# Kernel tuning notes

Measured on AMD Instinct MI355X. Metric: run time of the kernel, lower is better.

Reference implementation:

```python
import jax, jax.numpy as jnp
import numpy as np

DIM = 192; D_STATE = 16; D_CONV = 4; EXPAND = 2
D_INNER = EXPAND * DIM          # 384
DT_RANK = -(-DIM // 16)         # ceil(192/16) = 12
BSZ, T, H, W = 1, 16, 64, 64


def setup_inputs() -> dict:
    key = jax.random.key(0)
    ks = jax.random.split(key, 10)
    s = 0.02
    return {
        "x": jax.random.normal(ks[0], (BSZ, DIM, T, H, W), jnp.float32),
        "ln1_g": jnp.ones((DIM,), jnp.float32),
        "ln1_b": jnp.zeros((DIM,), jnp.float32),
        "ln2_g": jnp.ones((DIM,), jnp.float32),
        "ln2_b": jnp.zeros((DIM,), jnp.float32),
        "W_in": jax.random.normal(ks[1], (2 * D_INNER, DIM), jnp.float32) * s,
        "conv_w": jax.random.normal(ks[2], (D_INNER, D_CONV), jnp.float32) * 0.3,
        "conv_b": jnp.zeros((D_INNER,), jnp.float32),
        "W_xp": jax.random.normal(ks[3], (DT_RANK + 2 * D_STATE, D_INNER), jnp.float32) * s,
        "W_dt": jax.random.normal(ks[4], (D_INNER, DT_RANK), jnp.float32) * 0.1,
        "b_dt": jax.random.normal(ks[5], (D_INNER,), jnp.float32) * 0.1 - 4.0,
        "A_log": jnp.log(jnp.broadcast_to(jnp.arange(1, D_STATE + 1, dtype=jnp.float32), (D_INNER, D_STATE))),
        "D": jnp.ones((D_INNER,), jnp.float32),
        "W_out": jax.random.normal(ks[6], (DIM, D_INNER), jnp.float32) * s,
    }


def _layer_norm(x, g, b, eps=1e-5):
    m = x.mean(-1, keepdims=True)
    v = ((x - m) ** 2).mean(-1, keepdims=True)
    return (x - m) * jax.lax.rsqrt(v + eps) * g + b


def _mamba(tokens, W_in, conv_w, conv_b, W_xp, W_dt, b_dt, A_log, D, W_out):
    B, L, _ = tokens.shape
    xz = tokens @ W_in.T                      # (B, L, 2*d_inner)
    xc, z = jnp.split(xz, 2, axis=-1)
    # causal depthwise conv1d along L
    xin = xc.transpose(0, 2, 1)               # (B, d_inner, L)
    xconv = jax.lax.conv_general_dilated(
        xin, conv_w[:, None, :], (1,), [(D_CONV - 1, 0)],
        dimension_numbers=("NCH", "OIH", "NCH"), feature_group_count=D_INNER)
    xconv = xconv + conv_b[None, :, None]
    xs = jax.nn.silu(xconv.transpose(0, 2, 1))  # (B, L, d_inner)
    x_dbl = xs @ W_xp.T                        # (B, L, dt_rank + 2*d_state)
    dt, Bm, Cm = jnp.split(x_dbl, [DT_RANK, DT_RANK + D_STATE], axis=-1)
    dt = jax.nn.softplus(dt @ W_dt.T + b_dt)   # (B, L, d_inner)
    A = -jnp.exp(A_log)                        # (d_inner, d_state)
    dA = jnp.exp(dt[..., None] * A)            # (B, L, d_inner, d_state)
    dBx = dt[..., None] * Bm[:, :, None, :] * xs[..., None]

    def step(h, inp):
        dA_t, dBx_t, C_t = inp
        h = dA_t * h + dBx_t                   # (B, d_inner, d_state)
        return h, jnp.einsum("bds,bs->bd", h, C_t)

    h0 = jnp.zeros((B, D_INNER, D_STATE), tokens.dtype)
    _, ys = jax.lax.scan(step, h0, (dA.transpose(1, 0, 2, 3),
                                    dBx.transpose(1, 0, 2, 3),
                                    Cm.transpose(1, 0, 2)))
    y = ys.transpose(1, 0, 2) + xs * D         # (B, L, d_inner)
    y = y * jax.nn.silu(z)
    return y @ W_out.T                          # (B, L, dim)


def reference(x, ln1_g, ln1_b, ln2_g, ln2_b, W_in, conv_w, conv_b,
              W_xp, W_dt, b_dt, A_log, D, W_out):
    B, C, T_, H_, W_ = x.shape
    Hs, Ws = H_ // 4, W_ // 4
    # avg_pool3d kernel=(1,4,4) stride=(1,4,4)
    x_ds = x.reshape(B, C, T_, Hs, 4, Ws, 4).mean((4, 6))
    tokens = x_ds.reshape(B, C, T_ * Hs * Ws).transpose(0, 2, 1)  # (B, L, C)
    y = _layer_norm(tokens, ln1_g, ln1_b)
    y = _mamba(y, W_in, conv_w, conv_b, W_xp, W_dt, b_dt, A_log, D, W_out)
    out = _layer_norm(tokens + y, ln2_g, ln2_b)                    # (B, L, C)
    out5 = out.transpose(0, 2, 1).reshape(B, C, T_, Hs, Ws)
    pooled = out5.mean((3, 4))                                     # (B, C, T)
    mag = jnp.abs(jnp.fft.rfft(pooled, axis=2))
    weight = jax.nn.sigmoid(mag[:, :, 1:8].mean(-1))               # (B, C)
    out5 = out5 * weight[:, :, None, None, None]
    up = jax.image.resize(out5, (B, C, T_, H_, W_), method="trilinear")
    return up * jax.nn.sigmoid(x)
```

## Files before the change

kernel.cpp:

```cpp
#include <hip/hip_runtime.h>
#include <math.h>

#define DIMC 192
#define DI   384
#define DS   16
#define LTOK 4096
#define NCH  256
#define CLEN 16
#define NLANE (DI*DS)
#define L2E  1.4426950408889634f
#define LN2  0.6931471805599453f

typedef __attribute__((ext_vector_type(8))) short    bf16x8;
typedef __attribute__((ext_vector_type(8))) unsigned short u16x8;
typedef __attribute__((ext_vector_type(4))) float    f32x4;

__device__ __forceinline__ float EXP2(float x) { return __builtin_amdgcn_exp2f(x); }
__device__ __forceinline__ float RCP(float x)  { return __builtin_amdgcn_rcpf(x); }
__device__ __forceinline__ float LOG2(float x) { return __builtin_amdgcn_logf(x); }

__device__ __forceinline__ float sigmoidf_(float x) { return RCP(1.f + EXP2(-x * L2E)); }
__device__ __forceinline__ float siluf_(float x)    { return x * RCP(1.f + EXP2(-x * L2E)); }
__device__ __forceinline__ unsigned short f2bf(float f) {
    unsigned int u = __float_as_uint(f);
    u += 0x7FFFu + ((u >> 16) & 1u);
    return (unsigned short)(u >> 16);
}
__device__ __forceinline__ float bf2f(unsigned short b) {
    return __uint_as_float(((unsigned int)b) << 16);
}

__global__ __launch_bounds__(256) void poolln_kernel(const float* __restrict__ x,
                                                     const float* __restrict__ g,
                                                     const float* __restrict__ bb,
                                                     const float* __restrict__ W_in,
                                                     const float* __restrict__ W_out,
                                                     const float* __restrict__ W_xp,
                                                     const float* __restrict__ A_log,
                                                     float* __restrict__ tokens,
                                                     unsigned short* __restrict__ ytok,
                                                     unsigned short* __restrict__ W_in_bf,
                                                     unsigned short* __restrict__ W_out_bf,
                                                     unsigned short* __restrict__ W_xp_pad,
                                                     float* __restrict__ A2pre) {
    int blk = blockIdx.x;
    int tid = threadIdx.x;
    if (blk >= 256) {
        int id = (blk - 256) * 256 + tid;
        for (int i = id; i < 768 * 192; i += 8192) W_in_bf[i] = f2bf(W_in[i]);
        for (int i = id; i < 192 * 384; i += 8192) W_out_bf[i] = f2bf(W_out[i]);
        for (int i = id; i < 64 * 384; i += 8192) {
            int row = i / 384;
            W_xp_pad[i] = (row < 44) ? f2bf(W_xp[i]) : (unsigned short)0;
        }
        for (int i = id; i < NLANE; i += 8192) A2pre[i] = -expf(A_log[i]) * L2E;
        return;
    }
    int t = blk >> 4, hs = blk & 15;
    int grp = tid >> 4, ws = tid & 15;
    __shared__ float P[16 * 196];
    __shared__ float ms[16], rs[16];
    #pragma unroll
    for (int k = 0; k < 12; ++k) {
        int c = grp + (k << 4);
        const float* base = x + ((size_t)(c * 16 + t) * 64 + hs * 4) * 64 + ws * 4;
        float s = 0.f;
        #pragma unroll
        for (int i = 0; i < 4; ++i) {
            float4 v = *(const float4*)(base + i * 64);
            s += v.x + v.y + v.z + v.w;
        }
        P[ws * 196 + c] = s * 0.0625f;
    }
    __syncthreads();
    float s1 = 0.f, s2 = 0.f;
    #pragma unroll
    for (int k = 0; k < 12; ++k) {
        float v = P[grp * 196 + ws + 16 * k];
        s1 += v; s2 += v * v;
    }
    s1 += __shfl_xor(s1, 1); s2 += __shfl_xor(s2, 1);
    s1 += __shfl_xor(s1, 2); s2 += __shfl_xor(s2, 2);
    s1 += __shfl_xor(s1, 4); s2 += __shfl_xor(s2, 4);
    s1 += __shfl_xor(s1, 8); s2 += __shfl_xor(s2, 8);
    if (ws == 0) {
        float m = s1 * (1.f / 192.f);
        ms[grp] = m;
        rs[grp] = rsqrtf(s2 * (1.f / 192.f) - m * m + 1e-5f);
    }
    __syncthreads();
    int l0 = t * 256 + hs * 16;
    for (int e = tid; e < 16 * 192; e += 256) {
        int w2 = e / 192, c = e - w2 * 192;
        float v = P[w2 * 196 + c];
        float val = (v - ms[w2]) * rs[w2] * g[c] + bb[c];
        tokens[(size_t)(l0 + w2) * DIMC + c] = v;
        ytok[(size_t)(l0 + w2) * DIMC + c] = f2bf(val);
    }
}

template<int K>
__global__ __launch_bounds__(256) void gemm_mfma(const unsigned short* __restrict__ A,
                                                 const unsigned short* __restrict__ Wb,
                                                 float* __restrict__ Cout,
                                                 int N) {
    constexpr int KT = 192;
    constexpr int KP = KT + 8;
    __shared__ unsigned short As[64 * KP];
    __shared__ unsigned short Bs[64 * KP];
    int bm = blockIdx.y * 64;
    int bn = blockIdx.x * 64;
    int tid = threadIdx.x;
    int lane = tid & 63, w = tid >> 6;
    int wr = w >> 1, wc = w & 1;
    int r16 = lane & 15, h = lane >> 4;
    f32x4 acc[2][2] = {};
    for (int kt = 0; kt < K; kt += KT) {
        for (int c = tid; c < 64 * (KT / 8); c += 256) {
            int row = c / (KT / 8), col = (c % (KT / 8)) * 8;
            *(u16x8*)&As[row * KP + col] = *(const u16x8*)(A + (size_t)(bm + row) * K + kt + col);
            *(u16x8*)&Bs[row * KP + col] = *(const u16x8*)(Wb + (size_t)(bn + row) * K + kt + col);
        }
        __syncthreads();
        #pragma unroll
        for (int k0 = 0; k0 < KT; k0 += 32) {
            bf16x8 a0 = *(const bf16x8*)&As[(wr * 32 + r16)      * KP + k0 + 8 * h];
            bf16x8 a1 = *(const bf16x8*)&As[(wr * 32 + 16 + r16) * KP + k0 + 8 * h];
            bf16x8 b0 = *(const bf16x8*)&Bs[(wc * 32 + r16)      * KP + k0 + 8 * h];
            bf16x8 b1 = *(const bf16x8*)&Bs[(wc * 32 + 16 + r16) * KP + k0 + 8 * h];
            acc[0][0] = __builtin_amdgcn_mfma_f32_16x16x32_bf16(a0, b0, acc[0][0], 0, 0, 0);
            acc[0][1] = __builtin_amdgcn_mfma_f32_16x16x32_bf16(a0, b1, acc[0][1], 0, 0, 0);
            acc[1][0] = __builtin_amdgcn_mfma_f32_16x16x32_bf16(a1, b0, acc[1][0], 0, 0, 0);
            acc[1][1] = __builtin_amdgcn_mfma_f32_16x16x32_bf16(a1, b1, acc[1][1], 0, 0, 0);
        }
        __syncthreads();
    }
    #pragma unroll
    for (int fm = 0; fm < 2; ++fm)
        #pragma unroll
        for (int fn = 0; fn < 2; ++fn)
            #pragma unroll
            for (int i = 0; i < 4; ++i) {
                int r = bm + wr * 32 + fm * 16 + h * 4 + i;
                int cc = bn + wc * 32 + fn * 16 + r16;
                Cout[(size_t)r * N + cc] = acc[fm][fn][i];
            }
}

__global__ __launch_bounds__(256) void convxdbl(const float* __restrict__ xz,
                                                const float* __restrict__ conv_w,
                                                const float* __restrict__ conv_b,
                                                const unsigned short* __restrict__ Wxp,
                                                unsigned short* __restrict__ xsb,
                                                float* __restrict__ x_dbl) {
    int l0 = blockIdx.x * 16;
    int tid = threadIdx.x;
    __shared__ unsigned short As[16 * 392];
    __shared__ float xd[16 * 64];
    for (int e = tid * 2; e < 16 * 384; e += 512) {
        int row = e / 384, d = e - row * 384;
        int l = l0 + row;
        float ax = conv_b[d], ay = conv_b[d + 1];
        #pragma unroll
        for (int k = 0; k < 4; ++k) {
            int ll = l - 3 + k;
            if (ll >= 0) {
                float2 v = *(const float2*)(xz + (size_t)ll * 768 + d);
                ax = fmaf(conv_w[d * 4 + k],       v.x, ax);
                ay = fmaf(conv_w[(d + 1) * 4 + k], v.y, ay);
            }
        }
        ushort2 b2;
        b2.x = f2bf(siluf_(ax));
        b2.y = f2bf(siluf_(ay));
        *(ushort2*)&As[row * 392 + d] = b2;
        *(ushort2*)(xsb + (size_t)l * 384 + d) = b2;
    }
    __syncthreads();
    int lane = tid & 63, w = tid >> 6;
    int r16 = lane & 15, hh = lane >> 4;
    f32x4 acc = {};
    #pragma unroll
    for (int k0 = 0; k0 < 384; k0 += 32) {
        bf16x8 a = *(const bf16x8*)&As[r16 * 392 + k0 + 8 * hh];
        bf16x8 b = *(const bf16x8*)(Wxp + (size_t)(w * 16 + r16) * 384 + k0 + 8 * hh);
        acc = __builtin_amdgcn_mfma_f32_16x16x32_bf16(a, b, acc, 0, 0, 0);
    }
    #pragma unroll
    for (int i = 0; i < 4; ++i) xd[(hh * 4 + i) * 64 + w * 16 + r16] = acc[i];
    __syncthreads();
    {
        int e = tid * 4;
        int row = e >> 6, col = e & 63;
        *(float4*)(x_dbl + (size_t)(l0 + row) * 64 + col) = *(const float4*)&xd[e];
    }
}

__global__ __launch_bounds__(256) void scan1(const float* __restrict__ x_dbl,
                                             const unsigned short* __restrict__ xsb,
                                             const float* __restrict__ W_dt,
                                             const float* __restrict__ b_dt,
                                             const float* __restrict__ A2pre,
                                             float* __restrict__ chA,
                                             float* __restrict__ chB,
                                             float* __restrict__ Dloc,
                                             unsigned short* __restrict__ yloc) {
    int tid = threadIdx.x;
    int dg = blockIdx.x;
    int c  = blockIdx.y;
    __shared__ float xdblS[16 * 48];
    __shared__ float wdtS[64 * 13];
    __shared__ float dtS[16][64];
    __shared__ unsigned short xsS[16][64];
    for (int i = tid; i < 768; i += 256) {
        int row = i / 48, col = i - row * 48;
        xdblS[i] = x_dbl[(size_t)(c * 16 + row) * 64 + col];
    }
    for (int i = tid; i < 768; i += 256) {
        int dl_ = i / 12, r = i - dl_ * 12;
        wdtS[dl_ * 13 + r] = W_dt[(size_t)dg * 768 + i];
    }
    for (int i = tid; i < 1024; i += 256) {
        int row = i >> 6, dl_ = i & 63;
        xsS[row][dl_] = xsb[(size_t)(c * 16 + row) * 384 + dg * 64 + dl_];
    }
    __syncthreads();
    {
        int dl_ = tid & 63;
        float bd = b_dt[dg * 64 + dl_];
        #pragma unroll
        for (int i2 = 0; i2 < 4; ++i2) {
            int row = (tid >> 6) + 4 * i2;
            float s = bd;
            #pragma unroll
            for (int r = 0; r < 12; ++r)
                s = fmaf(xdblS[row * 48 + r], wdtS[dl_ * 13 + r], s);
            dtS[row][dl_] = (s > 20.f) ? s : LOG2(1.f + EXP2(s * L2E)) * LN2;
        }
    }
    __syncthreads();
    int sq = tid & 3, dl = tid >> 2;
    int d = dg * 64 + dl;
    float4 a4 = *(const float4*)(A2pre + (size_t)d * DS + sq * 4);
    float A2[4] = {a4.x, a4.y, a4.z, a4.w};
    float h[4] = {};
    float dts = 0.f;
    #pragma unroll
    for (int i = 0; i < CLEN; ++i) {
        int l = c * CLEN + i;
        float dtv = dtS[i][dl];
        float xv  = bf2f(xsS[i][dl]);
        float dtx = dtv * xv;
        dts += dtv;
        float y = 0.f;
        #pragma unroll
        for (int u = 0; u < 4; ++u) {
            float a = EXP2(dtv * A2[u]);
            h[u] = fmaf(a, h[u], dtx * xdblS[i * 48 + 12 + sq * 4 + u]);
            y = fmaf(h[u], xdblS[i * 48 + 28 + sq * 4 + u], y);
        }
        y += __shfl_xor(y, 1);
        y += __shfl_xor(y, 2);
        if (sq == 0) {
            yloc[(size_t)l * DI + d] = f2bf(y);
            Dloc[(size_t)l * DI + d] = dts;
        }
    }
    size_t base = (size_t)c * NLANE + d * DS + sq * 4;
    float4 pa, pb;
    pa.x = EXP2(dts * A2[0]); pa.y = EXP2(dts * A2[1]);
    pa.z = EXP2(dts * A2[2]); pa.w = EXP2(dts * A2[3]);
    pb.x = h[0]; pb.y = h[1]; pb.z = h[2]; pb.w = h[3];
    *(float4*)&chA[base] = pa;
    *(float4*)&chB[base] = pb;
}

__global__ __launch_bounds__(256) void scan2p(const float* __restrict__ chA,
                                              const float* __restrict__ chB,
                                              float* __restrict__ hst) {
    int tid = threadIdx.x;
    int ll = tid & 15;
    int g  = tid >> 4;
    int lane = blockIdx.x * 16 + ll;
    float a[16], b[16];
    #pragma unroll
    for (int i = 0; i < 16; ++i) {
        int c = g * 16 + i;
        a[i] = chA[(size_t)c * NLANE + lane];
        b[i] = chB[(size_t)c * NLANE + lane];
    }
    float Ath = 1.f, Bth = 0.f;
    #pragma unroll
    for (int i = 0; i < 16; ++i) {
        Bth = fmaf(a[i], Bth, b[i]);
        Ath *= a[i];
    }
    __shared__ float sA[16][17], sB[16][17];
    sA[g][ll] = Ath; sB[g][ll] = Bth;
    __syncthreads();
    #pragma unroll
    for (int step = 1; step < 16; step <<= 1) {
        float pA = 1.f, pB = 0.f;
        if (g >= step) { pA = sA[g - step][ll]; pB = sB[g - step][ll]; }
        __syncthreads();
        if (g >= step) {
            float cA = sA[g][ll], cB = sB[g][ll];
            sA[g][ll] = cA * pA;
            sB[g][ll] = fmaf(cA, pB, cB);
        }
        __syncthreads();
    }
    float h = (g == 0) ? 0.f : sB[g - 1][ll];
    #pragma unroll
    for (int i = 0; i < 16; ++i) {
        int c = g * 16 + i;
        hst[(size_t)c * NLANE + lane] = h;
        h = fmaf(a[i], h, b[i]);
    }
}

__global__ __launch_bounds__(256) void scan3fix(const float* __restrict__ hst,
                                                const float* __restrict__ Dloc,
                                                const float* __restrict__ x_dbl,
                                                const float* __restrict__ A2pre,
                                                const unsigned short* __restrict__ xsb,
                                                const float* __restrict__ xz,
                                                const float* __restrict__ Dvec,
                                                unsigned short* __restrict__ ybuf) {
    int dg = blockIdx.x;
    int c  = blockIdx.y;
    int tid = threadIdx.x;
    int ll = tid >> 4, dl = tid & 15;
    int d = dg * 16 + dl;
    int l = c * 16 + ll;
    __shared__ float hpS[16][17];
    __shared__ float A2S[16][17];
    __shared__ float CsS[256];
    {
        int dd = tid >> 4, ss = tid & 15;
        hpS[dd][ss] = hst[(size_t)c * NLANE + dg * 256 + tid];
        A2S[dd][ss] = A2pre[(size_t)dg * 256 + tid];
        CsS[tid]    = x_dbl[(size_t)(c * 16 + dd) * 64 + 28 + ss];
    }
    __syncthreads();
    float Dl = Dloc[(size_t)l * DI + d];
    float y  = bf2f(ybuf[(size_t)l * DI + d]);
    float xv = bf2f(xsb[(size_t)l * DI + d]);
    float z  = xz[(size_t)l * 768 + 384 + d];
    #pragma unroll
    for (int s = 0; s < 16; ++s) {
        float e = EXP2(A2S[dl][s] * Dl);
        y = fmaf(CsS[ll * 16 + s] * e, hpS[dl][s], y);
    }
    float val = (y + xv * Dvec[d]) * siluf_(z);
    ybuf[(size_t)l * DI + d] = f2bf(val);
}

__global__ __launch_bounds__(256) void ln2_kernel(const float* __restrict__ tokens,
                                                  const float* __restrict__ gout,
                                                  const float* __restrict__ g,
                                                  const float* __restrict__ bb,
                                                  float* __restrict__ o5) {
    int blk = blockIdx.x;
    int t = blk >> 4, g16 = blk & 15;
    int l0 = t * 256 + g16 * 16;
    int tid = threadIdx.x;
    __shared__ float P[16 * 196];
    __shared__ float ms[16], rs[16];
    for (int e = tid; e < 3072; e += 256) {
        int w2 = e / 192, c = e - w2 * 192;
        size_t off = (size_t)(l0 + w2) * DIMC + c;
        P[w2 * 196 + c] = tokens[off] + gout[off];
    }
    __syncthreads();
    int grp = tid >> 4, ws = tid & 15;
    float s1 = 0.f, s2 = 0.f;
    #pragma unroll
    for (int k = 0; k < 12; ++k) {
        float v = P[grp * 196 + ws + 16 * k];
        s1 += v; s2 += v * v;
    }
    s1 += __shfl_xor(s1, 1); s2 += __shfl_xor(s2, 1);
    s1 += __shfl_xor(s1, 2); s2 += __shfl_xor(s2, 2);
    s1 += __shfl_xor(s1, 4); s2 += __shfl_xor(s2, 4);
    s1 += __shfl_xor(s1, 8); s2 += __shfl_xor(s2, 8);
    if (ws == 0) {
        float m = s1 * (1.f / 192.f);
        ms[grp] = m;
        rs[grp] = rsqrtf(s2 * (1.f / 192.f) - m * m + 1e-5f);
    }
    __syncthreads();
    for (int e = tid; e < 3072; e += 256) {
        int c = e >> 4, w2 = e & 15;
        float val = (P[w2 * 196 + c] - ms[w2]) * rs[w2] * g[c] + bb[c];
        o5[((size_t)c * 16 + t) * 256 + g16 * 16 + w2] = val;
    }
}

__global__ __launch_bounds__(256) void fft_kernel(const float* __restrict__ o5,
                                                  float* __restrict__ wgt) {
    int c = blockIdx.x;
    __shared__ float pooled[16];
    __shared__ float mag[8];
    int tid = threadIdx.x;
    int wv = tid >> 6, lane = tid & 63;
    for (int t = wv * 4; t < wv * 4 + 4; ++t) {
        float s = 0.f;
        #pragma unroll
        for (int r = 0; r < 4; ++r) s += o5[(size_t)c * 4096 + t * 256 + lane + r * 64];
        s += __shfl_xor(s, 1); s += __shfl_xor(s, 2); s += __shfl_xor(s, 4);
        s += __shfl_xor(s, 8); s += __shfl_xor(s, 16); s += __shfl_xor(s, 32);
        if (lane == 0) pooled[t] = s * (1.f / 256.f);
    }
    __syncthreads();
    if (tid >= 1 && tid <= 7) {
        int k = tid;
        float re = 0.f, im = 0.f;
        for (int t = 0; t < 16; ++t) {
            float ang = -0.39269908169872414f * (float)(k * t);
            re = fmaf(pooled[t], cosf(ang), re);
            im = fmaf(pooled[t], sinf(ang), im);
        }
        mag[k] = sqrtf(re * re + im * im);
    }
    __syncthreads();
    if (tid == 0) {
        float m = 0.f;
        for (int k = 1; k <= 7; ++k) m += mag[k];
        wgt[c] = sigmoidf_(m * (1.f / 7.f));
    }
}

__global__ __launch_bounds__(256) void upsample_kernel(const float* __restrict__ o5,
                                                       const float* __restrict__ wgt,
                                                       const float* __restrict__ x,
                                                       float* __restrict__ out) {
    int idx = blockIdx.x * 256 + threadIdx.x;
    int k  = idx & 15;
    int h  = (idx >> 4) & 63;
    int t  = (idx >> 10) & 15;
    int c  = idx >> 14;
    float sh = h * 0.25f - 0.375f;
    int h0 = (int)floorf(sh); float fh = sh - (float)h0;
    int h0c = min(max(h0, 0), 15), h1c = min(max(h0 + 1, 0), 15);
    const float* pl = o5 + ((size_t)c * 16 + t) * 256;
    int cm = max(k - 1, 0), cp = min(k + 1, 15);
    float r0m = pl[h0c * 16 + cm], r00 = pl[h0c * 16 + k], r0p = pl[h0c * 16 + cp];
    float r1m = pl[h1c * 16 + cm], r10 = pl[h1c * 16 + k], r1p = pl[h1c * 16 + cp];
    float gh = 1.f - fh;
    float vm = r0m * gh + r1m * fh;
    float v0 = r00 * gh + r10 * fh;
    float vp = r0p * gh + r1p * fh;
    float wc = wgt[c];
    size_t off = (size_t)idx * 4;
    float4 xv = *(const float4*)(x + off);
    float4 o;
    o.x = (vm * 0.375f + v0 * 0.625f) * wc * sigmoidf_(xv.x);
    o.y = (vm * 0.125f + v0 * 0.875f) * wc * sigmoidf_(xv.y);
    o.z = (v0 * 0.875f + vp * 0.125f) * wc * sigmoidf_(xv.z);
    o.w = (v0 * 0.625f + vp * 0.375f) * wc * sigmoidf_(xv.w);
    *(float4*)(out + off) = o;
}

extern "C" void kernel_launch(void* const* d_in, const int* in_sizes, int n_in,
                              void* d_out, int out_size, void* d_ws, size_t ws_size,
                              hipStream_t stream) {
    const float* x      = (const float*)d_in[0];
    const float* ln1_g  = (const float*)d_in[1];
    const float* ln1_b  = (const float*)d_in[2];
    const float* ln2_g  = (const float*)d_in[3];
    const float* ln2_b  = (const float*)d_in[4];
    const float* W_in   = (const float*)d_in[5];
    const float* conv_w = (const float*)d_in[6];
    const float* conv_b = (const float*)d_in[7];
    const float* W_xp   = (const float*)d_in[8];
    const float* W_dt   = (const float*)d_in[9];
    const float* b_dt   = (const float*)d_in[10];
    const float* A_log  = (const float*)d_in[11];
    const float* Dvec   = (const float*)d_in[12];
    const float* W_out  = (const float*)d_in[13];
    float* out = (float*)d_out;

    float* ws = (float*)d_ws;
    float* tokens = ws;  ws += (size_t)LTOK * DIMC;
    float* xz     = ws;  ws += (size_t)LTOK * 768;
    float* x_dbl  = ws;  ws += (size_t)LTOK * 64;
    float* chA    = ws;  ws += (size_t)NLANE * NCH;
    float* chB    = ws;  ws += (size_t)NLANE * NCH;
    float* hst    = ws;  ws += (size_t)NLANE * NCH;
    float* Dloc   = ws;  ws += (size_t)LTOK * DI;
    float* gout   = ws;  ws += (size_t)LTOK * DIMC;
    float* o5     = ws;  ws += (size_t)DIMC * LTOK;
    float* A2pre  = ws;  ws += NLANE;
    float* wgt    = ws;  ws += 256;
    unsigned short* ytok     = (unsigned short*)ws;  ws += (size_t)LTOK * DIMC / 2;
    unsigned short* ybuf     = (unsigned short*)ws;  ws += (size_t)LTOK * DI / 2;
    unsigned short* xsb      = (unsigned short*)ws;  ws += (size_t)LTOK * DI / 2;
    unsigned short* W_in_bf  = (unsigned short*)ws;  ws += (size_t)768 * 192 / 2;
    unsigned short* W_out_bf = (unsigned short*)ws;  ws += (size_t)192 * 384 / 2;
    unsigned short* W_xp_pad = (unsigned short*)ws;  ws += (size_t)64 * 384 / 2;

    poolln_kernel<<<288, 256, 0, stream>>>(x, ln1_g, ln1_b, W_in, W_out, W_xp, A_log,
                                           tokens, ytok, W_in_bf, W_out_bf, W_xp_pad, A2pre);
    gemm_mfma<192><<<dim3(12, 64), 256, 0, stream>>>(ytok, W_in_bf, xz, 768);
    convxdbl<<<256, 256, 0, stream>>>(xz, conv_w, conv_b, W_xp_pad, xsb, x_dbl);
    scan1<<<dim3(6, NCH), 256, 0, stream>>>(x_dbl, xsb, W_dt, b_dt, A2pre, chA, chB, Dloc, ybuf);
    scan2p<<<NLANE / 16, 256, 0, stream>>>(chA, chB, hst);
    scan3fix<<<dim3(24, NCH), 256, 0, stream>>>(hst, Dloc, x_dbl, A2pre, xsb, xz, Dvec, ybuf);
    gemm_mfma<384><<<dim3(3, 64), 256, 0, stream>>>(ybuf, W_out_bf, gout, 192);
    ln2_kernel<<<256, 256, 0, stream>>>(tokens, gout, ln2_g, ln2_b, o5);
    fft_kernel<<<192, 256, 0, stream>>>(o5, wgt);
    upsample_kernel<<<12288, 256, 0, stream>>>(o5, wgt, x, out);
}
```

Before: 116.0 us.

## Fuse conv+xproj with chunk scan, out-GEMM with LN2, and FFT with upsample

Merges the conv/x-projection kernel with the first scan pass into one 384-thread block per chunk, where each thread owns one channel and all 16 states, so x_dbl and xs are reused from shared memory. It also fuses the output projection GEMM with the residual-add and second LayerNorm, which drops the gout buffer. The per-channel FFT gating is recomputed inside each upsample block, removing two launches and the wgt buffer. In exchange, the scan gets fewer and larger blocks (256 blocks), the gemmln kernel runs only 64 blocks, and the pooled FFT work is repeated 16 times per channel.

```diff
diff --git a/kernel.cpp b/kernel.cpp
--- a/kernel.cpp
+++ b/kernel.cpp
@@ -147,132 +147,113 @@
             }
 }
 
-__global__ __launch_bounds__(256) void convxdbl(const float* __restrict__ xz,
+__global__ __launch_bounds__(384) void convscan(const float* __restrict__ xz,
                                                 const float* __restrict__ conv_w,
                                                 const float* __restrict__ conv_b,
                                                 const unsigned short* __restrict__ Wxp,
+                                                const float* __restrict__ W_dt,
+                                                const float* __restrict__ b_dt,
+                                                const float* __restrict__ A2pre,
                                                 unsigned short* __restrict__ xsb,
-                                                float* __restrict__ x_dbl) {
-    int l0 = blockIdx.x * 16;
+                                                float* __restrict__ x_dbl,
+                                                float* __restrict__ chA,
+                                                float* __restrict__ chB,
+                                                float* __restrict__ Dloc,
+                                                unsigned short* __restrict__ yloc) {
+    int c = blockIdx.x;
+    int l0 = c * CLEN;
     int tid = threadIdx.x;
     __shared__ unsigned short As[16 * 392];
     __shared__ float xd[16 * 64];
-    for (int e = tid * 2; e < 16 * 384; e += 512) {
-        int row = e / 384, d = e - row * 384;
-        int l = l0 + row;
-        float ax = conv_b[d], ay = conv_b[d + 1];
-        #pragma unroll
-        for (int k = 0; k < 4; ++k) {
-            int ll = l - 3 + k;
-            if (ll >= 0) {
-                float2 v = *(const float2*)(xz + (size_t)ll * 768 + d);
-                ax = fmaf(conv_w[d * 4 + k],       v.x, ax);
-                ay = fmaf(conv_w[(d + 1) * 4 + k], v.y, ay);
-            }
-        }
-        ushort2 b2;
-        b2.x = f2bf(siluf_(ax));
-        b2.y = f2bf(siluf_(ay));
-        *(ushort2*)&As[row * 392 + d] = b2;
-        *(ushort2*)(xsb + (size_t)l * 384 + d) = b2;
-    }
-    __syncthreads();
-    int lane = tid & 63, w = tid >> 6;
-    int r16 = lane & 15, hh = lane >> 4;
-    f32x4 acc = {};
-    #pragma unroll
-    for (int k0 = 0; k0 < 384; k0 += 32) {
-        bf16x8 a = *(const bf16x8*)&As[r16 * 392 + k0 + 8 * hh];
-        bf16x8 b = *(const bf16x8*)(Wxp + (size_t)(w * 16 + r16) * 384 + k0 + 8 * hh);
-        acc = __builtin_amdgcn_mfma_f32_16x16x32_bf16(a, b, acc, 0, 0, 0);
-    }
-    #pragma unroll
-    for (int i = 0; i < 4; ++i) xd[(hh * 4 + i) * 64 + w * 16 + r16] = acc[i];
-    __syncthreads();
     {
-        int e = tid * 4;
-        int row = e >> 6, col = e & 63;
-        *(float4*)(x_dbl + (size_t)(l0 + row) * 64 + col) = *(const float4*)&xd[e];
-    }
-}
-
-__global__ __launch_bounds__(256) void scan1(const float* __restrict__ x_dbl,
-                                             const unsigned short* __restrict__ xsb,
-                                             const float* __restrict__ W_dt,
-                                             const float* __restrict__ b_dt,
-                                             const float* __restrict__ A2pre,
-                                             float* __restrict__ chA,
-                                             float* __restrict__ chB,
-                                             float* __restrict__ Dloc,
-                                             unsigned short* __restrict__ yloc) {
-    int tid = threadIdx.x;
-    int dg = blockIdx.x;
-    int c  = blockIdx.y;
-    __shared__ float xdblS[16 * 48];
-    __shared__ float wdtS[64 * 13];
-    __shared__ float dtS[16][64];
-    __shared__ unsigned short xsS[16][64];
-    for (int i = tid; i < 768; i += 256) {
-        int row = i / 48, col = i - row * 48;
-        xdblS[i] = x_dbl[(size_t)(c * 16 + row) * 64 + col];
-    }
-    for (int i = tid; i < 768; i += 256) {
-        int dl_ = i / 12, r = i - dl_ * 12;
-        wdtS[dl_ * 13 + r] = W_dt[(size_t)dg * 768 + i];
-    }
-    for (int i = tid; i < 1024; i += 256) {
-        int row = i >> 6, dl_ = i & 63;
-        xsS[row][dl_] = xsb[(size_t)(c * 16 + row) * 384 + dg * 64 + dl_];
-    }
-    __syncthreads();
-    {
-        int dl_ = tid & 63;
-        float bd = b_dt[dg * 64 + dl_];
-        #pragma unroll
-        for (int i2 = 0; i2 < 4; ++i2) {
-            int row = (tid >> 6) + 4 * i2;
-            float s = bd;
-            #pragma unroll
-            for (int r = 0; r < 12; ++r)
-                s = fmaf(xdblS[row * 48 + r], wdtS[dl_ * 13 + r], s);
-            dtS[row][dl_] = (s > 20.f) ? s : LOG2(1.f + EXP2(s * L2E)) * LN2;
-        }
-    }
-    __syncthreads();
-    int sq = tid & 3, dl = tid >> 2;
-    int d = dg * 64 + dl;
-    float4 a4 = *(const float4*)(A2pre + (size_t)d * DS + sq * 4);
-    float A2[4] = {a4.x, a4.y, a4.z, a4.w};
-    float h[4] = {};
+        int d = tid;
+        float cw0 = conv_w[d * 4 + 0], cw1 = conv_w[d * 4 + 1];
+        float cw2 = conv_w[d * 4 + 2], cw3 = conv_w[d * 4 + 3];
+        float cb = conv_b[d];
+        float xv[19];
+        #pragma unroll
+        for (int j = 0; j < 19; ++j) {
+            int ll = l0 - 3 + j;
+            xv[j] = (ll >= 0) ? xz[(size_t)ll * 768 + d] : 0.f;
+        }
+        #pragma unroll
+        for (int i = 0; i < 16; ++i) {
+            float a = cb;
+            a = fmaf(cw0, xv[i], a);
+            a = fmaf(cw1, xv[i + 1], a);
+            a = fmaf(cw2, xv[i + 2], a);
+            a = fmaf(cw3, xv[i + 3], a);
+            As[i * 392 + d] = f2bf(siluf_(a));
+        }
+    }
+    __syncthreads();
+    #pragma unroll
+    for (int k = 0; k < 16; ++k)
+        xsb[(size_t)(l0 + k) * DI + tid] = As[k * 392 + tid];
+    if (tid < 256) {
+        int lane = tid & 63, w = tid >> 6;
+        int r16 = lane & 15, hh = lane >> 4;
+        f32x4 acc = {};
+        #pragma unroll
+        for (int k0 = 0; k0 < 384; k0 += 32) {
+            bf16x8 a = *(const bf16x8*)&As[r16 * 392 + k0 + 8 * hh];
+            bf16x8 b = *(const bf16x8*)(Wxp + (size_t)(w * 16 + r16) * 384 + k0 + 8 * hh);
+            acc = __builtin_amdgcn_mfma_f32_16x16x32_bf16(a, b, acc, 0, 0, 0);
+        }
+        #pragma unroll
+        for (int i = 0; i < 4; ++i) xd[(hh * 4 + i) * 64 + w * 16 + r16] = acc[i];
+    }
+    __syncthreads();
+    if (tid < 256) {
+        int row = tid >> 6, col = (tid & 63) * 4;
+        *(float4*)(x_dbl + (size_t)(l0 + row) * 64 + col) = *(const float4*)&xd[row * 64 + col];
+        *(float4*)(x_dbl + (size_t)(l0 + 4 + row) * 64 + col) = *(const float4*)&xd[(4 + row) * 64 + col];
+        *(float4*)(x_dbl + (size_t)(l0 + 8 + row) * 64 + col) = *(const float4*)&xd[(8 + row) * 64 + col];
+        *(float4*)(x_dbl + (size_t)(l0 + 12 + row) * 64 + col) = *(const float4*)&xd[(12 + row) * 64 + col];
+    }
+    int d = tid;
+    float wdt[12];
+    #pragma unroll
+    for (int r = 0; r < 12; ++r) wdt[r] = W_dt[d * 12 + r];
+    float bd = b_dt[d];
+    float A2[16];
+    #pragma unroll
+    for (int s = 0; s < 16; s += 4) {
+        float4 a4 = *(const float4*)(A2pre + (size_t)d * DS + s);
+        A2[s] = a4.x; A2[s + 1] = a4.y; A2[s + 2] = a4.z; A2[s + 3] = a4.w;
+    }
+    float h[16] = {};
     float dts = 0.f;
     #pragma unroll
     for (int i = 0; i < CLEN; ++i) {
-        int l = c * CLEN + i;
-        float dtv = dtS[i][dl];
-        float xv  = bf2f(xsS[i][dl]);
-        float dtx = dtv * xv;
+        float sdt = bd;
+        #pragma unroll
+        for (int r = 0; r < 12; ++r) sdt = fmaf(xd[i * 64 + r], wdt[r], sdt);
+        float dtv = (sdt > 20.f) ? sdt : LOG2(1.f + EXP2(sdt * L2E)) * LN2;
+        float xvv = bf2f(As[i * 392 + d]);
+        float dtx = dtv * xvv;
         dts += dtv;
         float y = 0.f;
         #pragma unroll
-        for (int u = 0; u < 4; ++u) {
-            float a = EXP2(dtv * A2[u]);
-            h[u] = fmaf(a, h[u], dtx * xdblS[i * 48 + 12 + sq * 4 + u]);
-            y = fmaf(h[u], xdblS[i * 48 + 28 + sq * 4 + u], y);
-        }
-        y += __shfl_xor(y, 1);
-        y += __shfl_xor(y, 2);
-        if (sq == 0) {
-            yloc[(size_t)l * DI + d] = f2bf(y);
-            Dloc[(size_t)l * DI + d] = dts;
-        }
-    }
-    size_t base = (size_t)c * NLANE + d * DS + sq * 4;
-    float4 pa, pb;
-    pa.x = EXP2(dts * A2[0]); pa.y = EXP2(dts * A2[1]);
-    pa.z = EXP2(dts * A2[2]); pa.w = EXP2(dts * A2[3]);
-    pb.x = h[0]; pb.y = h[1]; pb.z = h[2]; pb.w = h[3];
-    *(float4*)&chA[base] = pa;
-    *(float4*)&chB[base] = pb;
+        for (int s = 0; s < 16; ++s) {
+            float a = EXP2(dtv * A2[s]);
+            h[s] = fmaf(a, h[s], dtx * xd[i * 64 + 12 + s]);
+            y = fmaf(h[s], xd[i * 64 + 28 + s], y);
+        }
+        int l = l0 + i;
+        yloc[(size_t)l * DI + d] = f2bf(y);
+        Dloc[(size_t)l * DI + d] = dts;
+    }
+    size_t base = (size_t)c * NLANE + d * DS;
+    #pragma unroll
+    for (int s = 0; s < 16; s += 4) {
+        float4 pa, pb;
+        pa.x = EXP2(dts * A2[s + 0]); pa.y = EXP2(dts * A2[s + 1]);
+        pa.z = EXP2(dts * A2[s + 2]); pa.w = EXP2(dts * A2[s + 3]);
+        pb.x = h[s + 0]; pb.y = h[s + 1]; pb.z = h[s + 2]; pb.w = h[s + 3];
+        *(float4*)&chA[base + s] = pa;
+        *(float4*)&chB[base + s] = pb;
+    }
 }
 
 __global__ __launch_bounds__(256) void scan2p(const float* __restrict__ chA,
@@ -356,70 +337,114 @@
     ybuf[(size_t)l * DI + d] = f2bf(val);
 }
 
-__global__ __launch_bounds__(256) void ln2_kernel(const float* __restrict__ tokens,
-                                                  const float* __restrict__ gout,
-                                                  const float* __restrict__ g,
-                                                  const float* __restrict__ bb,
-                                                  float* __restrict__ o5) {
+__global__ __launch_bounds__(256) void gemmln(const unsigned short* __restrict__ A,
+                                              const unsigned short* __restrict__ Wb,
+                                              const float* __restrict__ tokens,
+                                              const float* __restrict__ g,
+                                              const float* __restrict__ bb,
+                                              float* __restrict__ o5) {
+    constexpr int K = 384, KT = 192, KP = KT + 8;
+    __shared__ char smem[(64 + 192) * KP * 2];
+    unsigned short* As = (unsigned short*)smem;
+    unsigned short* Bs = As + 64 * KP;
+    float* P = (float*)smem;
+    __shared__ float ms[64], rs[64];
+    int bm = blockIdx.x * 64;
+    int tid = threadIdx.x;
+    int lane = tid & 63, w = tid >> 6;
+    int r16 = lane & 15, hh = lane >> 4;
+    f32x4 acc[12] = {};
+    for (int kt = 0; kt < K; kt += KT) {
+        for (int cc = tid; cc < 64 * (KT / 8); cc += 256) {
+            int row = cc / (KT / 8), col = (cc % (KT / 8)) * 8;
+            *(u16x8*)&As[row * KP + col] = *(const u16x8*)(A + (size_t)(bm + row) * K + kt + col);
+        }
+        for (int cc = tid; cc < 192 * (KT / 8); cc += 256) {
+            int row = cc / (KT / 8), col = (cc % (KT / 8)) * 8;
+            *(u16x8*)&Bs[row * KP + col] = *(const u16x8*)(Wb + (size_t)row * K + kt + col);
+        }
+        __syncthreads();
+        #pragma unroll
+        for (int k0 = 0; k0 < KT; k0 += 32) {
+            bf16x8 a = *(const bf16x8*)&As[(w * 16 + r16) * KP + k0 + 8 * hh];
+            #pragma unroll
+            for (int j = 0; j < 12; ++j) {
+                bf16x8 b = *(const bf16x8*)&Bs[(j * 16 + r16) * KP + k0 + 8 * hh];
+                acc[j] = __builtin_amdgcn_mfma_f32_16x16x32_bf16(a, b, acc[j], 0, 0, 0);
+            }
+        }
+        __syncthreads();
+    }
+    for (int e = tid; e < 64 * 192; e += 256) {
+        int row = e / 192, col = e - row * 192;
+        P[row * 193 + col] = tokens[(size_t)(bm + row) * DIMC + col];
+    }
+    __syncthreads();
+    #pragma unroll
+    for (int j = 0; j < 12; ++j)
+        #pragma unroll
+        for (int i = 0; i < 4; ++i)
+            P[(w * 16 + hh * 4 + i) * 193 + j * 16 + r16] += acc[j][i];
+    __syncthreads();
+    {
+        int tk = tid >> 2, q = tid & 3;
+        float s1 = 0.f, s2 = 0.f;
+        #pragma unroll
+        for (int u = 0; u < 48; ++u) {
+            float v = P[tk * 193 + q * 48 + u];
+            s1 += v; s2 += v * v;
+        }
+        s1 += __shfl_xor(s1, 1); s2 += __shfl_xor(s2, 1);
+        s1 += __shfl_xor(s1, 2); s2 += __shfl_xor(s2, 2);
+        if (q == 0) {
+            float m = s1 * (1.f / 192.f);
+            ms[tk] = m;
+            rs[tk] = rsqrtf(s2 * (1.f / 192.f) - m * m + 1e-5f);
+        }
+    }
+    __syncthreads();
+    int t = bm >> 8;
+    int sp0 = bm & 255;
+    for (int e = tid; e < 64 * 192; e += 256) {
+        int cch = e >> 6, row = e & 63;
+        float val = (P[row * 193 + cch] - ms[row]) * rs[row] * g[cch] + bb[cch];
+        o5[(size_t)cch * 4096 + t * 256 + sp0 + row] = val;
+    }
+}
+
+__global__ __launch_bounds__(256) void upfft(const float* __restrict__ o5,
+                                             const float* __restrict__ x,
+                                             float* __restrict__ out) {
     int blk = blockIdx.x;
-    int t = blk >> 4, g16 = blk & 15;
-    int l0 = t * 256 + g16 * 16;
-    int tid = threadIdx.x;
-    __shared__ float P[16 * 196];
-    __shared__ float ms[16], rs[16];
-    for (int e = tid; e < 3072; e += 256) {
-        int w2 = e / 192, c = e - w2 * 192;
-        size_t off = (size_t)(l0 + w2) * DIMC + c;
-        P[w2 * 196 + c] = tokens[off] + gout[off];
-    }
-    __syncthreads();
-    int grp = tid >> 4, ws = tid & 15;
-    float s1 = 0.f, s2 = 0.f;
-    #pragma unroll
-    for (int k = 0; k < 12; ++k) {
-        float v = P[grp * 196 + ws + 16 * k];
-        s1 += v; s2 += v * v;
-    }
-    s1 += __shfl_xor(s1, 1); s2 += __shfl_xor(s2, 1);
-    s1 += __shfl_xor(s1, 2); s2 += __shfl_xor(s2, 2);
-    s1 += __shfl_xor(s1, 4); s2 += __shfl_xor(s2, 4);
-    s1 += __shfl_xor(s1, 8); s2 += __shfl_xor(s2, 8);
-    if (ws == 0) {
-        float m = s1 * (1.f / 192.f);
-        ms[grp] = m;
-        rs[grp] = rsqrtf(s2 * (1.f / 192.f) - m * m + 1e-5f);
-    }
-    __syncthreads();
-    for (int e = tid; e < 3072; e += 256) {
-        int c = e >> 4, w2 = e & 15;
-        float val = (P[w2 * 196 + c] - ms[w2]) * rs[w2] * g[c] + bb[c];
-        o5[((size_t)c * 16 + t) * 256 + g16 * 16 + w2] = val;
-    }
-}
-
-__global__ __launch_bounds__(256) void fft_kernel(const float* __restrict__ o5,
-                                                  float* __restrict__ wgt) {
-    int c = blockIdx.x;
+    int c = blk >> 4, t = blk & 15;
+    int tid = threadIdx.x;
+    __shared__ float pl[256];
     __shared__ float pooled[16];
     __shared__ float mag[8];
-    int tid = threadIdx.x;
+    __shared__ float wgt_s;
     int wv = tid >> 6, lane = tid & 63;
-    for (int t = wv * 4; t < wv * 4 + 4; ++t) {
+    #pragma unroll
+    for (int rr = 0; rr < 4; ++rr) {
+        int r = wv * 4 + rr;
         float s = 0.f;
         #pragma unroll
-        for (int r = 0; r < 4; ++r) s += o5[(size_t)c * 4096 + t * 256 + lane + r * 64];
+        for (int u = 0; u < 4; ++u) {
+            float v = o5[(size_t)c * 4096 + r * 256 + lane + u * 64];
+            s += v;
+            if (r == t) pl[lane + u * 64] = v;
+        }
         s += __shfl_xor(s, 1); s += __shfl_xor(s, 2); s += __shfl_xor(s, 4);
         s += __shfl_xor(s, 8); s += __shfl_xor(s, 16); s += __shfl_xor(s, 32);
-        if (lane == 0) pooled[t] = s * (1.f / 256.f);
+        if (lane == 0) pooled[r] = s * (1.f / 256.f);
     }
     __syncthreads();
     if (tid >= 1 && tid <= 7) {
         int k = tid;
         float re = 0.f, im = 0.f;
-        for (int t = 0; t < 16; ++t) {
-            float ang = -0.39269908169872414f * (float)(k * t);
-            re = fmaf(pooled[t], cosf(ang), re);
-            im = fmaf(pooled[t], sinf(ang), im);
+        for (int tt = 0; tt < 16; ++tt) {
+            float ang = -0.39269908169872414f * (float)(k * tt);
+            re = fmaf(pooled[tt], cosf(ang), re);
+            im = fmaf(pooled[tt], sinf(ang), im);
         }
         mag[k] = sqrtf(re * re + im * im);
     }
@@ -427,39 +452,35 @@
     if (tid == 0) {
         float m = 0.f;
         for (int k = 1; k <= 7; ++k) m += mag[k];
-        wgt[c] = sigmoidf_(m * (1.f / 7.f));
-    }
-}
-
-__global__ __launch_bounds__(256) void upsample_kernel(const float* __restrict__ o5,
-                                                       const float* __restrict__ wgt,
-                                                       const float* __restrict__ x,
-                                                       float* __restrict__ out) {
-    int idx = blockIdx.x * 256 + threadIdx.x;
-    int k  = idx & 15;
-    int h  = (idx >> 4) & 63;
-    int t  = (idx >> 10) & 15;
-    int c  = idx >> 14;
-    float sh = h * 0.25f - 0.375f;
-    int h0 = (int)floorf(sh); float fh = sh - (float)h0;
-    int h0c = min(max(h0, 0), 15), h1c = min(max(h0 + 1, 0), 15);
-    const float* pl = o5 + ((size_t)c * 16 + t) * 256;
-    int cm = max(k - 1, 0), cp = min(k + 1, 15);
-    float r0m = pl[h0c * 16 + cm], r00 = pl[h0c * 16 + k], r0p = pl[h0c * 16 + cp];
-    float r1m = pl[h1c * 16 + cm], r10 = pl[h1c * 16 + k], r1p = pl[h1c * 16 + cp];
-    float gh = 1.f - fh;
-    float vm = r0m * gh + r1m * fh;
-    float v0 = r00 * gh + r10 * fh;
-    float vp = r0p * gh + r1p * fh;
-    float wc = wgt[c];
-    size_t off = (size_t)idx * 4;
-    float4 xv = *(const float4*)(x + off);
-    float4 o;
-    o.x = (vm * 0.375f + v0 * 0.625f) * wc * sigmoidf_(xv.x);
-    o.y = (vm * 0.125f + v0 * 0.875f) * wc * sigmoidf_(xv.y);
-    o.z = (v0 * 0.875f + vp * 0.125f) * wc * sigmoidf_(xv.z);
-    o.w = (v0 * 0.625f + vp * 0.375f) * wc * sigmoidf_(xv.w);
-    *(float4*)(out + off) = o;
+        wgt_s = sigmoidf_(m * (1.f / 7.f));
+    }
+    __syncthreads();
+    float wc = wgt_s;
+    size_t planeoff = (size_t)blk * 4096;
+    #pragma unroll
+    for (int p = 0; p < 4; ++p) {
+        int px4 = p * 256 + tid;
+        int k = px4 & 15;
+        int hrow = px4 >> 4;
+        float sh = hrow * 0.25f - 0.375f;
+        int h0 = (int)floorf(sh); float fh = sh - (float)h0;
+        int h0c = min(max(h0, 0), 15), h1c = min(max(h0 + 1, 0), 15);
+        int cm = max(k - 1, 0), cp = min(k + 1, 15);
+        float r0m = pl[h0c * 16 + cm], r00 = pl[h0c * 16 + k], r0p = pl[h0c * 16 + cp];
+        float r1m = pl[h1c * 16 + cm], r10 = pl[h1c * 16 + k], r1p = pl[h1c * 16 + cp];
+        float gh = 1.f - fh;
+        float vm = r0m * gh + r1m * fh;
+        float v0 = r00 * gh + r10 * fh;
+        float vp = r0p * gh + r1p * fh;
+        size_t off = planeoff + (size_t)px4 * 4;
+        float4 xv = *(const float4*)(x + off);
+        float4 o;
+        o.x = (vm * 0.375f + v0 * 0.625f) * wc * sigmoidf_(xv.x);
+        o.y = (vm * 0.125f + v0 * 0.875f) * wc * sigmoidf_(xv.y);
+        o.z = (v0 * 0.875f + vp * 0.125f) * wc * sigmoidf_(xv.z);
+        o.w = (v0 * 0.625f + vp * 0.375f) * wc * sigmoidf_(xv.w);
+        *(float4*)(out + off) = o;
+    }
 }
 
 extern "C" void kernel_launch(void* const* d_in, const int* in_sizes, int n_in,
@@ -489,10 +510,8 @@
     float* chB    = ws;  ws += (size_t)NLANE * NCH;
     float* hst    = ws;  ws += (size_t)NLANE * NCH;
     float* Dloc   = ws;  ws += (size_t)LTOK * DI;
-    float* gout   = ws;  ws += (size_t)LTOK * DIMC;
     float* o5     = ws;  ws += (size_t)DIMC * LTOK;
     float* A2pre  = ws;  ws += NLANE;
-    float* wgt    = ws;  ws += 256;
     unsigned short* ytok     = (unsigned short*)ws;  ws += (size_t)LTOK * DIMC / 2;
     unsigned short* ybuf     = (unsigned short*)ws;  ws += (size_t)LTOK * DI / 2;
     unsigned short* xsb      = (unsigned short*)ws;  ws += (size_t)LTOK * DI / 2;
@@ -503,12 +522,10 @@
     poolln_kernel<<<288, 256, 0, stream>>>(x, ln1_g, ln1_b, W_in, W_out, W_xp, A_log,
                                            tokens, ytok, W_in_bf, W_out_bf, W_xp_pad, A2pre);
     gemm_mfma<192><<<dim3(12, 64), 256, 0, stream>>>(ytok, W_in_bf, xz, 768);
-    convxdbl<<<256, 256, 0, stream>>>(xz, conv_w, conv_b, W_xp_pad, xsb, x_dbl);
-    scan1<<<dim3(6, NCH), 256, 0, stream>>>(x_dbl, xsb, W_dt, b_dt, A2pre, chA, chB, Dloc, ybuf);
+    convscan<<<NCH, 384, 0, stream>>>(xz, conv_w, conv_b, W_xp_pad, W_dt, b_dt, A2pre,
+                                      xsb, x_dbl, chA, chB, Dloc, ybuf);
     scan2p<<<NLANE / 16, 256, 0, stream>>>(chA, chB, hst);
     scan3fix<<<dim3(24, NCH), 256, 0, stream>>>(hst, Dloc, x_dbl, A2pre, xsb, xz, Dvec, ybuf);
-    gemm_mfma<384><<<dim3(3, 64), 256, 0, stream>>>(ybuf, W_out_bf, gout, 192);
-    ln2_kernel<<<256, 256, 0, stream>>>(tokens, gout, ln2_g, ln2_b, o5);
-    fft_kernel<<<192, 256, 0, stream>>>(o5, wgt);
-    upsample_kernel<<<12288, 256, 0, stream>>>(o5, wgt, x, out);
-}
+    gemmln<<<64, 256, 0, stream>>>(ybuf, W_out_bf, tokens, ln2_g, ln2_b, o5);
+    upfft<<<3072, 256, 0, stream>>>(o5, x, out);
+}
```

Result: faster. 112.9 us (-2.7%).

## Fuse out-projection GEMM with residual LayerNorm, and FFT gating with upsample

Applied to the files above, without the earlier changes.

Merges the W_out GEMM, residual add and second LayerNorm into one kernel, so the gout intermediate is never written to global memory. Also folds the per-channel FFT weight computation into the upsample kernel: each block recomputes its channel's pooled spectrum and stages its plane in shared memory. This drops two launches and a round trip through global memory. In exchange, the fused GEMM runs on only 64 blocks, which leaves much of the GPU idle, and the FFT reduction is recomputed 16 times per channel.

```diff
diff --git a/kernel.cpp b/kernel.cpp
--- a/kernel.cpp
+++ b/kernel.cpp
@@ -356,70 +356,114 @@
     ybuf[(size_t)l * DI + d] = f2bf(val);
 }
 
-__global__ __launch_bounds__(256) void ln2_kernel(const float* __restrict__ tokens,
-                                                  const float* __restrict__ gout,
-                                                  const float* __restrict__ g,
-                                                  const float* __restrict__ bb,
-                                                  float* __restrict__ o5) {
+__global__ __launch_bounds__(256) void gemmln(const unsigned short* __restrict__ A,
+                                              const unsigned short* __restrict__ Wb,
+                                              const float* __restrict__ tokens,
+                                              const float* __restrict__ g,
+                                              const float* __restrict__ bb,
+                                              float* __restrict__ o5) {
+    constexpr int K = 384, KT = 192, KP = KT + 8;
+    __shared__ char smem[(64 + 192) * KP * 2];
+    unsigned short* As = (unsigned short*)smem;
+    unsigned short* Bs = As + 64 * KP;
+    float* P = (float*)smem;
+    __shared__ float ms[64], rs[64];
+    int bm = blockIdx.x * 64;
+    int tid = threadIdx.x;
+    int lane = tid & 63, w = tid >> 6;
+    int r16 = lane & 15, hh = lane >> 4;
+    f32x4 acc[12] = {};
+    for (int kt = 0; kt < K; kt += KT) {
+        for (int cc = tid; cc < 64 * (KT / 8); cc += 256) {
+            int row = cc / (KT / 8), col = (cc % (KT / 8)) * 8;
+            *(u16x8*)&As[row * KP + col] = *(const u16x8*)(A + (size_t)(bm + row) * K + kt + col);
+        }
+        for (int cc = tid; cc < 192 * (KT / 8); cc += 256) {
+            int row = cc / (KT / 8), col = (cc % (KT / 8)) * 8;
+            *(u16x8*)&Bs[row * KP + col] = *(const u16x8*)(Wb + (size_t)row * K + kt + col);
+        }
+        __syncthreads();
+        #pragma unroll
+        for (int k0 = 0; k0 < KT; k0 += 32) {
+            bf16x8 a = *(const bf16x8*)&As[(w * 16 + r16) * KP + k0 + 8 * hh];
+            #pragma unroll
+            for (int j = 0; j < 12; ++j) {
+                bf16x8 b = *(const bf16x8*)&Bs[(j * 16 + r16) * KP + k0 + 8 * hh];
+                acc[j] = __builtin_amdgcn_mfma_f32_16x16x32_bf16(a, b, acc[j], 0, 0, 0);
+            }
+        }
+        __syncthreads();
+    }
+    for (int e = tid; e < 64 * 192; e += 256) {
+        int row = e / 192, col = e - row * 192;
+        P[row * 193 + col] = tokens[(size_t)(bm + row) * DIMC + col];
+    }
+    __syncthreads();
+    #pragma unroll
+    for (int j = 0; j < 12; ++j)
+        #pragma unroll
+        for (int i = 0; i < 4; ++i)
+            P[(w * 16 + hh * 4 + i) * 193 + j * 16 + r16] += acc[j][i];
+    __syncthreads();
+    {
+        int tk = tid >> 2, q = tid & 3;
+        float s1 = 0.f, s2 = 0.f;
+        #pragma unroll
+        for (int u = 0; u < 48; ++u) {
+            float v = P[tk * 193 + q * 48 + u];
+            s1 += v; s2 += v * v;
+        }
+        s1 += __shfl_xor(s1, 1); s2 += __shfl_xor(s2, 1);
+        s1 += __shfl_xor(s1, 2); s2 += __shfl_xor(s2, 2);
+        if (q == 0) {
+            float m = s1 * (1.f / 192.f);
+            ms[tk] = m;
+            rs[tk] = rsqrtf(s2 * (1.f / 192.f) - m * m + 1e-5f);
+        }
+    }
+    __syncthreads();
+    int t = bm >> 8;
+    int sp0 = bm & 255;
+    for (int e = tid; e < 64 * 192; e += 256) {
+        int cch = e >> 6, row = e & 63;
+        float val = (P[row * 193 + cch] - ms[row]) * rs[row] * g[cch] + bb[cch];
+        o5[(size_t)cch * 4096 + t * 256 + sp0 + row] = val;
+    }
+}
+
+__global__ __launch_bounds__(256) void upfft(const float* __restrict__ o5,
+                                             const float* __restrict__ x,
+                                             float* __restrict__ out) {
     int blk = blockIdx.x;
-    int t = blk >> 4, g16 = blk & 15;
-    int l0 = t * 256 + g16 * 16;
-    int tid = threadIdx.x;
-    __shared__ float P[16 * 196];
-    __shared__ float ms[16], rs[16];
-    for (int e = tid; e < 3072; e += 256) {
-        int w2 = e / 192, c = e - w2 * 192;
-        size_t off = (size_t)(l0 + w2) * DIMC + c;
-        P[w2 * 196 + c] = tokens[off] + gout[off];
-    }
-    __syncthreads();
-    int grp = tid >> 4, ws = tid & 15;
-    float s1 = 0.f, s2 = 0.f;
-    #pragma unroll
-    for (int k = 0; k < 12; ++k) {
-        float v = P[grp * 196 + ws + 16 * k];
-        s1 += v; s2 += v * v;
-    }
-    s1 += __shfl_xor(s1, 1); s2 += __shfl_xor(s2, 1);
-    s1 += __shfl_xor(s1, 2); s2 += __shfl_xor(s2, 2);
-    s1 += __shfl_xor(s1, 4); s2 += __shfl_xor(s2, 4);
-    s1 += __shfl_xor(s1, 8); s2 += __shfl_xor(s2, 8);
-    if (ws == 0) {
-        float m = s1 * (1.f / 192.f);
-        ms[grp] = m;
-        rs[grp] = rsqrtf(s2 * (1.f / 192.f) - m * m + 1e-5f);
-    }
-    __syncthreads();
-    for (int e = tid; e < 3072; e += 256) {
-        int c = e >> 4, w2 = e & 15;
-        float val = (P[w2 * 196 + c] - ms[w2]) * rs[w2] * g[c] + bb[c];
-        o5[((size_t)c * 16 + t) * 256 + g16 * 16 + w2] = val;
-    }
-}
-
-__global__ __launch_bounds__(256) void fft_kernel(const float* __restrict__ o5,
-                                                  float* __restrict__ wgt) {
-    int c = blockIdx.x;
+    int c = blk >> 4, t = blk & 15;
+    int tid = threadIdx.x;
+    __shared__ float pl[256];
     __shared__ float pooled[16];
     __shared__ float mag[8];
-    int tid = threadIdx.x;
+    __shared__ float wgt_s;
     int wv = tid >> 6, lane = tid & 63;
-    for (int t = wv * 4; t < wv * 4 + 4; ++t) {
+    #pragma unroll
+    for (int rr = 0; rr < 4; ++rr) {
+        int r = wv * 4 + rr;
         float s = 0.f;
         #pragma unroll
-        for (int r = 0; r < 4; ++r) s += o5[(size_t)c * 4096 + t * 256 + lane + r * 64];
+        for (int u = 0; u < 4; ++u) {
+            float v = o5[(size_t)c * 4096 + r * 256 + lane + u * 64];
+            s += v;
+            if (r == t) pl[lane + u * 64] = v;
+        }
         s += __shfl_xor(s, 1); s += __shfl_xor(s, 2); s += __shfl_xor(s, 4);
         s += __shfl_xor(s, 8); s += __shfl_xor(s, 16); s += __shfl_xor(s, 32);
-        if (lane == 0) pooled[t] = s * (1.f / 256.f);
+        if (lane == 0) pooled[r] = s * (1.f / 256.f);
     }
     __syncthreads();
     if (tid >= 1 && tid <= 7) {
         int k = tid;
         float re = 0.f, im = 0.f;
-        for (int t = 0; t < 16; ++t) {
-            float ang = -0.39269908169872414f * (float)(k * t);
-            re = fmaf(pooled[t], cosf(ang), re);
-            im = fmaf(pooled[t], sinf(ang), im);
+        for (int tt = 0; tt < 16; ++tt) {
+            float ang = -0.39269908169872414f * (float)(k * tt);
+            re = fmaf(pooled[tt], cosf(ang), re);
+            im = fmaf(pooled[tt], sinf(ang), im);
         }
         mag[k] = sqrtf(re * re + im * im);
     }
@@ -427,39 +471,35 @@
     if (tid == 0) {
         float m = 0.f;
         for (int k = 1; k <= 7; ++k) m += mag[k];
-        wgt[c] = sigmoidf_(m * (1.f / 7.f));
-    }
-}
-
-__global__ __launch_bounds__(256) void upsample_kernel(const float* __restrict__ o5,
-                                                       const float* __restrict__ wgt,
-                                                       const float* __restrict__ x,
-                                                       float* __restrict__ out) {
-    int idx = blockIdx.x * 256 + threadIdx.x;
-    int k  = idx & 15;
-    int h  = (idx >> 4) & 63;
-    int t  = (idx >> 10) & 15;
-    int c  = idx >> 14;
-    float sh = h * 0.25f - 0.375f;
-    int h0 = (int)floorf(sh); float fh = sh - (float)h0;
-    int h0c = min(max(h0, 0), 15), h1c = min(max(h0 + 1, 0), 15);
-    const float* pl = o5 + ((size_t)c * 16 + t) * 256;
-    int cm = max(k - 1, 0), cp = min(k + 1, 15);
-    float r0m = pl[h0c * 16 + cm], r00 = pl[h0c * 16 + k], r0p = pl[h0c * 16 + cp];
-    float r1m = pl[h1c * 16 + cm], r10 = pl[h1c * 16 + k], r1p = pl[h1c * 16 + cp];
-    float gh = 1.f - fh;
-    float vm = r0m * gh + r1m * fh;
-    float v0 = r00 * gh + r10 * fh;
-    float vp = r0p * gh + r1p * fh;
-    float wc = wgt[c];
-    size_t off = (size_t)idx * 4;
-    float4 xv = *(const float4*)(x + off);
-    float4 o;
-    o.x = (vm * 0.375f + v0 * 0.625f) * wc * sigmoidf_(xv.x);
-    o.y = (vm * 0.125f + v0 * 0.875f) * wc * sigmoidf_(xv.y);
-    o.z = (v0 * 0.875f + vp * 0.125f) * wc * sigmoidf_(xv.z);
-    o.w = (v0 * 0.625f + vp * 0.375f) * wc * sigmoidf_(xv.w);
-    *(float4*)(out + off) = o;
+        wgt_s = sigmoidf_(m * (1.f / 7.f));
+    }
+    __syncthreads();
+    float wc = wgt_s;
+    size_t planeoff = (size_t)blk * 4096;
+    #pragma unroll
+    for (int p = 0; p < 4; ++p) {
+        int px4 = p * 256 + tid;
+        int k = px4 & 15;
+        int hrow = px4 >> 4;
+        float sh = hrow * 0.25f - 0.375f;
+        int h0 = (int)floorf(sh); float fh = sh - (float)h0;
+        int h0c = min(max(h0, 0), 15), h1c = min(max(h0 + 1, 0), 15);
+        int cm = max(k - 1, 0), cp = min(k + 1, 15);
+        float r0m = pl[h0c * 16 + cm], r00 = pl[h0c * 16 + k], r0p = pl[h0c * 16 + cp];
+        float r1m = pl[h1c * 16 + cm], r10 = pl[h1c * 16 + k], r1p = pl[h1c * 16 + cp];
+        float gh = 1.f - fh;
+        float vm = r0m * gh + r1m * fh;
+        float v0 = r00 * gh + r10 * fh;
+        float vp = r0p * gh + r1p * fh;
+        size_t off = planeoff + (size_t)px4 * 4;
+        float4 xv = *(const float4*)(x + off);
+        float4 o;
+        o.x = (vm * 0.375f + v0 * 0.625f) * wc * sigmoidf_(xv.x);
+        o.y = (vm * 0.125f + v0 * 0.875f) * wc * sigmoidf_(xv.y);
+        o.z = (v0 * 0.875f + vp * 0.125f) * wc * sigmoidf_(xv.z);
+        o.w = (v0 * 0.625f + vp * 0.375f) * wc * sigmoidf_(xv.w);
+        *(float4*)(out + off) = o;
+    }
 }
 
 extern "C" void kernel_launch(void* const* d_in, const int* in_sizes, int n_in,
@@ -489,10 +529,8 @@
     float* chB    = ws;  ws += (size_t)NLANE * NCH;
     float* hst    = ws;  ws += (size_t)NLANE * NCH;
     float* Dloc   = ws;  ws += (size_t)LTOK * DI;
-    float* gout   = ws;  ws += (size_t)LTOK * DIMC;
     float* o5     = ws;  ws += (size_t)DIMC * LTOK;
     float* A2pre  = ws;  ws += NLANE;
-    float* wgt    = ws;  ws += 256;
     unsigned short* ytok     = (unsigned short*)ws;  ws += (size_t)LTOK * DIMC / 2;
     unsigned short* ybuf     = (unsigned short*)ws;  ws += (size_t)LTOK * DI / 2;
     unsigned short* xsb      = (unsigned short*)ws;  ws += (size_t)LTOK * DI / 2;
@@ -507,8 +545,6 @@
     scan1<<<dim3(6, NCH), 256, 0, stream>>>(x_dbl, xsb, W_dt, b_dt, A2pre, chA, chB, Dloc, ybuf);
     scan2p<<<NLANE / 16, 256, 0, stream>>>(chA, chB, hst);
     scan3fix<<<dim3(24, NCH), 256, 0, stream>>>(hst, Dloc, x_dbl, A2pre, xsb, xz, Dvec, ybuf);
-    gemm_mfma<384><<<dim3(3, 64), 256, 0, stream>>>(ybuf, W_out_bf, gout, 192);
-    ln2_kernel<<<256, 256, 0, stream>>>(tokens, gout, ln2_g, ln2_b, o5);
-    fft_kernel<<<192, 256, 0, stream>>>(o5, wgt);
-    upsample_kernel<<<12288, 256, 0, stream>>>(o5, wgt, x, out);
-}
+    gemmln<<<64, 256, 0, stream>>>(ybuf, W_out_bf, tokens, ln2_g, ln2_b, o5);
+    upfft<<<3072, 256, 0, stream>>>(o5, x, out);
+}
```

Result: slower. 131.0 us (+12.9%).
